# Kernel optimization log

Hardware: AMD Instinct MI355X
Metric: run time of the kernel (lower is better)

## Reference

```python
import jax, jax.numpy as jnp
import numpy as np

N, C_IN, C_OUT, T, V = 32, 4, 64, 6, 512


def setup_inputs() -> dict:
    key = jax.random.key(0)
    ks = jax.random.split(key, 8)
    x = jax.random.normal(ks[0], (N, C_IN, T, V), dtype=jnp.float32)
    # A carries 7 (unused) adjacency channels + 1 binary mask channel
    A = jax.random.randint(ks[1], (N, 8, V, V), 0, 2, dtype=jnp.int32)
    conv_w = jax.random.normal(ks[2], (C_OUT, C_IN), dtype=jnp.float32) / np.sqrt(C_IN).astype(np.float32)
    conv_b = jax.random.normal(ks[3], (C_OUT,), dtype=jnp.float32) * 0.02
    l2_w = jax.random.normal(ks[4], (1, T), dtype=jnp.float32) / np.sqrt(T).astype(np.float32)
    l2_b = jax.random.normal(ks[5], (1,), dtype=jnp.float32) * 0.02
    l1_w = jax.random.normal(ks[6], (1, 2 * C_OUT), dtype=jnp.float32) / np.sqrt(2 * C_OUT).astype(np.float32)
    l1_b = jax.random.normal(ks[7], (1,), dtype=jnp.float32) * 0.02
    return {"x": x, "A": A, "conv_w": conv_w, "conv_b": conv_b,
            "l2_w": l2_w, "l2_b": l2_b, "l1_w": l1_w, "l1_b": l1_b}


def reference(x, A, conv_w, conv_b, l2_w, l2_b, l1_w, l1_b):
    c = conv_w.shape[0]
    # 1x1 conv over (t, v): pure channel mix
    xc = jnp.einsum('nctv,oc->notv', x, conv_w) + conv_b[None, :, None, None]  # (n, 64, t, v)
    # temporal squeeze via l2: Linear(6 -> 1) on last (t) axis
    x1 = jnp.einsum('nctv,t->nvc', xc, l2_w[0]) + l2_b[0]  # (n, v, 64)
    # GAT-style pairwise score: l1(cat(x1_i, x1_j)) decomposes into two rank-1 terms
    e_i = x1 @ l1_w[0, :c]   # (n, v)
    e_j = x1 @ l1_w[0, c:]   # (n, v)
    scores = e_i[:, :, None] + e_j[:, None, :] + l1_b[0]  # (n, v, v), [n,i,j]
    scores = jnp.where(scores >= 0, scores, 0.2 * scores)  # LeakyReLU(0.2)
    # mask channel: A[:,7]; mask.long()==0 -> -inf
    mask = A[:, 7]  # (n, v, v) int
    scores = jnp.where(mask == 0, -jnp.inf, scores)
    p = jax.nn.softmax(scores, axis=2)
    p = jnp.where(jnp.isnan(p), 0.0, p)  # fully-masked rows -> 0
    # aggregate: nctv,ndvw->nctw with d=1
    out = jnp.einsum('nctv,nvw->nctw', xc, p)
    return out, p[:, None]  # (n, 64, t, v), (n, 1, v, v)
```

## Files before the change

### kernel.cpp

```cpp
#include <hip/hip_runtime.h>
#include <hip/hip_bf16.h>
#include <math.h>

#define NB   32
#define CIN  4
#define COUT 64
#define TT   6
#define VV   512
#define P_OFF (NB*COUT*TT*VV)
#define SPLITS 8
#define CH   (VV/SPLITS)
#define NROW 24
#define PKW  516

typedef __attribute__((ext_vector_type(8))) short bf16x8;
typedef __attribute__((ext_vector_type(4))) float f32x4;

__device__ inline unsigned int pack2(float a, float b) {
    __hip_bfloat162 h = __float22bfloat162_rn(make_float2(a, b));
    return *reinterpret_cast<unsigned int*>(&h);
}

__global__ __launch_bounds__(512, 4) void fused_kernel(
    const float* __restrict__ x,
    const int*   __restrict__ A,
    const float* __restrict__ conv_w,
    const float* __restrict__ conv_b,
    const float* __restrict__ l2_w,
    const float* __restrict__ l2_b,
    const float* __restrict__ l1_w,
    const float* __restrict__ l1_b,
    float*       __restrict__ p,
    float*       __restrict__ ypart)
{
    __shared__ float xst[CH][33];
    __shared__ unsigned int pk[16][PKW];
    __shared__ float W1s[CIN], W2s[CIN], cst[2], l2s[TT];
    __shared__ float ejl[VV];
    __shared__ float eil[CH];

    int s = blockIdx.x;
    int n = blockIdx.y;
    int tid = threadIdx.x;
    int lane = tid & 63;
    int q = tid >> 6;

    const int* mbase = A + (size_t)(n*8 + 7)*VV*VV;

    int4 mA0, mA1, mB0, mB1;
    {
        int i0 = s*CH + q*2;
        const int* mr = mbase + (size_t)i0*VV + lane*8;
        mA0 = *(const int4*)mr;       mA1 = *(const int4*)(mr + 4);
        mB0 = *(const int4*)(mr+VV);  mB1 = *(const int4*)(mr + VV + 4);
    }

    if (tid < CIN) {
        float w1 = 0.f, w2 = 0.f;
        for (int o = 0; o < COUT; ++o) {
            w1 += l1_w[o]        * conv_w[o*CIN + tid];
            w2 += l1_w[COUT + o] * conv_w[o*CIN + tid];
        }
        W1s[tid] = w1; W2s[tid] = w2;
    }
    if (tid < TT) l2s[tid] = l2_w[tid];
    if (tid == CIN) {
        float B1 = 0.f, B2 = 0.f, S1 = 0.f, S2 = 0.f;
        for (int o = 0; o < COUT; ++o) {
            B1 += l1_w[o]        * conv_b[o];
            B2 += l1_w[COUT + o] * conv_b[o];
            S1 += l1_w[o];
            S2 += l1_w[COUT + o];
        }
        float Ls = 0.f;
        for (int t = 0; t < TT; ++t) Ls += l2_w[t];
        cst[0] = Ls*B1 + l2_b[0]*S1;
        cst[1] = Ls*B2 + l2_b[0]*S2 + l1_b[0];
    }
    __syncthreads();

    {
        int j = tid;
        float ei = cst[0], ej = cst[1];
        #pragma unroll
        for (int c = 0; c < CIN; ++c) {
            float w1 = W1s[c], w2 = W2s[c];
            #pragma unroll
            for (int t = 0; t < TT; ++t) {
                float lw = l2s[t];
                float xv = x[((size_t)(n*CIN + c)*TT + t)*VV + j];
                ei = fmaf(lw*w1, xv, ei);
                ej = fmaf(lw*w2, xv, ej);
            }
        }
        ejl[j] = ej;
        if ((j >> 6) == s) eil[j & 63] = ei;
    }

    for (int idx = tid; idx < CH*33; idx += 512) {
        int r = idx >> 6;
        int i = idx & 63;
        float v = 0.f;
        if (r < NROW)       v = x[((size_t)n*NROW + r)*VV + s*CH + i];
        else if (r == NROW) v = 1.f;
        xst[i][r] = v;
    }
    __syncthreads();

    float ejv[8];
    #pragma unroll
    for (int m = 0; m < 8; ++m) ejv[m] = ejl[lane*8 + m];

    f32x4 acc[2][4];
    #pragma unroll
    for (int mt = 0; mt < 2; ++mt)
        #pragma unroll
        for (int t = 0; t < 4; ++t) acc[mt][t] = (f32x4){0.f, 0.f, 0.f, 0.f};

    bf16x8 afr[2][2];

    for (int sub = 0; sub < 4; ++sub) {
        int ilA  = sub*16 + q*2;
        int i_gA = s*CH + ilA;

        int4 cA0 = mA0, cA1 = mA1, cB0 = mB0, cB1 = mB1;
        float biasA = eil[ilA], biasB = eil[ilA + 1];

        if (sub < 3) {
            const int* mr = mbase + (size_t)(i_gA + 16)*VV + lane*8;
            mA0 = *(const int4*)mr;       mA1 = *(const int4*)(mr + 4);
            mB0 = *(const int4*)(mr+VV);  mB1 = *(const int4*)(mr + VV + 4);
        }

        float svA[8], svB[8];
        int mkA[8] = {cA0.x,cA0.y,cA0.z,cA0.w, cA1.x,cA1.y,cA1.z,cA1.w};
        int mkB[8] = {cB0.x,cB0.y,cB0.z,cB0.w, cB1.x,cB1.y,cB1.z,cB1.w};
        #pragma unroll
        for (int m2 = 0; m2 < 8; ++m2) {
            float tA = biasA + ejv[m2]; tA = (tA >= 0.f) ? tA : 0.2f*tA;
            svA[m2] = (mkA[m2] == 0) ? -INFINITY : tA;
            float tB = biasB + ejv[m2]; tB = (tB >= 0.f) ? tB : 0.2f*tB;
            svB[m2] = (mkB[m2] == 0) ? -INFINITY : tB;
        }
        float mA = svA[0], mB = svB[0];
        #pragma unroll
        for (int m2 = 1; m2 < 8; ++m2) {
            mA = fmaxf(mA, svA[m2]); mB = fmaxf(mB, svB[m2]);
        }
        #pragma unroll
        for (int off = 32; off; off >>= 1) {
            mA = fmaxf(mA, __shfl_xor(mA, off));
            mB = fmaxf(mB, __shfl_xor(mB, off));
        }
        float sumA = 0.f, sumB = 0.f;
        if (mA > -INFINITY) {
            #pragma unroll
            for (int m2 = 0; m2 < 8; ++m2) { svA[m2] = __expf(svA[m2]-mA); sumA += svA[m2]; }
        } else {
            #pragma unroll
            for (int m2 = 0; m2 < 8; ++m2) svA[m2] = 0.f;
        }
        if (mB > -INFINITY) {
            #pragma unroll
            for (int m2 = 0; m2 < 8; ++m2) { svB[m2] = __expf(svB[m2]-mB); sumB += svB[m2]; }
        } else {
            #pragma unroll
            for (int m2 = 0; m2 < 8; ++m2) svB[m2] = 0.f;
        }
        #pragma unroll
        for (int off = 32; off; off >>= 1) {
            sumA += __shfl_xor(sumA, off);
            sumB += __shfl_xor(sumB, off);
        }
        float invA = (sumA > 0.f) ? 1.f/sumA : 0.f;
        float invB = (sumB > 0.f) ? 1.f/sumB : 0.f;
        #pragma unroll
        for (int m2 = 0; m2 < 8; ++m2) { svA[m2] *= invA; svB[m2] *= invB; }

        float* prA = p + ((size_t)(n*VV + i_gA))*VV + lane*8;
        float4 pA03 = {svA[0],svA[1],svA[2],svA[3]}, pA47 = {svA[4],svA[5],svA[6],svA[7]};
        float4 pB03 = {svB[0],svB[1],svB[2],svB[3]}, pB47 = {svB[4],svB[5],svB[6],svB[7]};
        *(float4*)prA            = pA03;
        *(float4*)(prA + 4)      = pA47;
        *(float4*)(prA + VV)     = pB03;
        *(float4*)(prA + VV + 4) = pB47;

        {
            int pr = (sub & 1)*8 + q;
            uint4 u0 = {pack2(svA[0],svB[0]), pack2(svA[1],svB[1]),
                        pack2(svA[2],svB[2]), pack2(svA[3],svB[3])};
            uint4 u1 = {pack2(svA[4],svB[4]), pack2(svA[5],svB[5]),
                        pack2(svA[6],svB[6]), pack2(svA[7],svB[7])};
            *(uint4*)&pk[pr][lane*8]     = u0;
            *(uint4*)&pk[pr][lane*8 + 4] = u1;
        }

        if (sub & 1) {
            __syncthreads();

            if (sub == 1) {
                #pragma unroll
                for (int g = 0; g < 2; ++g)
                    #pragma unroll
                    for (int mt = 0; mt < 2; ++mt) {
                        int r  = mt*16 + (lane & 15);
                        int kb = g*32 + (lane >> 4)*8;
                        union { unsigned int u[4]; bf16x8 v; } ua;
                        #pragma unroll
                        for (int t = 0; t < 4; ++t)
                            ua.u[t] = pack2(xst[kb + 2*t][r], xst[kb + 2*t + 1][r]);
                        afr[g][mt] = ua.v;
                    }
            }

            int g = sub >> 1;
            #pragma unroll
            for (int t = 0; t < 4; ++t) {
                int ncol = (q*4 + t)*16 + (lane & 15);
                union { unsigned int u[4]; bf16x8 v; } ub;
                #pragma unroll
                for (int jj = 0; jj < 4; ++jj)
                    ub.u[jj] = pk[(lane >> 4)*4 + jj][ncol];
                acc[0][t] = __builtin_amdgcn_mfma_f32_16x16x32_bf16(afr[g][0], ub.v, acc[0][t], 0, 0, 0);
                acc[1][t] = __builtin_amdgcn_mfma_f32_16x16x32_bf16(afr[g][1], ub.v, acc[1][t], 0, 0, 0);
            }
            if (sub == 1) __syncthreads();
        }
    }

    float* yo = ypart + (size_t)(s*NB + n)*25*VV;
    #pragma unroll
    for (int mt = 0; mt < 2; ++mt)
        #pragma unroll
        for (int t = 0; t < 4; ++t) {
            int ncol = (q*4 + t)*16 + (lane & 15);
            #pragma unroll
            for (int reg = 0; reg < 4; ++reg) {
                int row = mt*16 + (lane >> 4)*4 + reg;
                if (row < 25)
                    yo[(size_t)row*VV + ncol] = acc[mt][t][reg];
            }
        }
}

__global__ __launch_bounds__(256) void expand_kernel(
    const float* __restrict__ ypart,
    const float* __restrict__ conv_w,
    const float* __restrict__ conv_b,
    float*       __restrict__ out)
{
    __shared__ float ysm[25][32];
    __shared__ float wsm[COUT*CIN];
    __shared__ float bsm[COUT];

    int wc = blockIdx.x;
    int n  = blockIdx.y;
    int tid = threadIdx.x;

    if (tid < COUT*CIN) wsm[tid] = conv_w[tid];
    if (tid < COUT)     bsm[tid] = conv_b[tid];

    for (int l4 = tid; l4 < 200; l4 += 256) {
        int r = l4 >> 3, w8 = l4 & 7;
        float4 a = {0.f, 0.f, 0.f, 0.f};
        #pragma unroll
        for (int s = 0; s < SPLITS; ++s) {
            float4 v = *(const float4*)(ypart +
                ((size_t)(s*NB + n)*25 + r)*VV + wc*32 + w8*4);
            a.x += v.x; a.y += v.y; a.z += v.z; a.w += v.w;
        }
        *(float4*)&ysm[r][w8*4] = a;
    }
    __syncthreads();

    int w  = tid & 31;
    int og = tid >> 5;

    float y[25];
    #pragma unroll
    for (int r = 0; r < 25; ++r) y[r] = ysm[r][w];

    #pragma unroll
    for (int oo = 0; oo < 8; ++oo) {
        int o = og*8 + oo;
        float wb[CIN];
        #pragma unroll
        for (int c = 0; c < CIN; ++c) wb[c] = wsm[o*CIN + c];
        float bo = bsm[o];
        #pragma unroll
        for (int t = 0; t < TT; ++t) {
            float val = bo * y[24];
            #pragma unroll
            for (int c = 0; c < CIN; ++c) val = fmaf(wb[c], y[c*TT + t], val);
            out[((size_t)(n*COUT + o)*TT + t)*VV + wc*32 + w] = val;
        }
    }
}

extern "C" void kernel_launch(void* const* d_in, const int* in_sizes, int n_in,
                              void* d_out, int out_size, void* d_ws, size_t ws_size,
                              hipStream_t stream)
{
    const float* x      = (const float*)d_in[0];
    const int*   A      = (const int*)  d_in[1];
    const float* conv_w = (const float*)d_in[2];
    const float* conv_b = (const float*)d_in[3];
    const float* l2_w   = (const float*)d_in[4];
    const float* l2_b   = (const float*)d_in[5];
    const float* l1_w   = (const float*)d_in[6];
    const float* l1_b   = (const float*)d_in[7];

    float* out = (float*)d_out;
    float* pP  = out + P_OFF;
    float* yp  = (float*)d_ws;

    dim3 gf(SPLITS, NB);
    fused_kernel<<<gf, 512, 0, stream>>>(x, A, conv_w, conv_b, l2_w, l2_b,
                                         l1_w, l1_b, pP, yp);

    dim3 ge(16, NB);
    expand_kernel<<<ge, 256, 0, stream>>>(yp, conv_w, conv_b, out);
}
```

Before: 33.60 us.

## Fuse expand kernel into main kernel via per-batch atomic counter barrier

Removes the separate expand kernel launch by having each of the 8 split blocks per batch signal completion through an atomic counter, spin-wait until all splits finish, then each block reduces the partial sums and expands two 32-column chunks of the output. This eliminates a kernel launch and its gap, but adds a memset launch and a spin-wait grid barrier that depends on all 256 blocks being co-resident. The extra shared memory may reduce occupancy.

Result: slower. 60.60 us (+80.4%).

```diff
diff --git a/kernel.cpp b/kernel.cpp
--- a/kernel.cpp
+++ b/kernel.cpp
@@ -31,13 +31,18 @@
     const float* __restrict__ l1_w,
     const float* __restrict__ l1_b,
     float*       __restrict__ p,
-    float*       __restrict__ ypart)
+    float*       __restrict__ ypart,
+    unsigned int* __restrict__ cnt,
+    float*       __restrict__ out)
 {
     __shared__ float xst[CH][33];
     __shared__ unsigned int pk[16][PKW];
     __shared__ float W1s[CIN], W2s[CIN], cst[2], l2s[TT];
     __shared__ float ejl[VV];
     __shared__ float eil[CH];
+    __shared__ float ysm[2][25][32];
+    __shared__ float wsm[COUT*CIN];
+    __shared__ float bsm[COUT];
 
     int s = blockIdx.x;
     int n = blockIdx.y;
@@ -55,6 +60,8 @@
         mB0 = *(const int4*)(mr+VV);  mB1 = *(const int4*)(mr + VV + 4);
     }
 
+    if (tid < COUT*CIN) wsm[tid] = conv_w[tid];
+    if (tid >= COUT*CIN && tid < COUT*CIN + COUT) bsm[tid - COUT*CIN] = conv_b[tid - COUT*CIN];
     if (tid < CIN) {
         float w1 = 0.f, w2 = 0.f;
         for (int o = 0; o < COUT; ++o) {
@@ -241,58 +248,56 @@
                     yo[(size_t)row*VV + ncol] = acc[mt][t][reg];
             }
         }
-}
-
-__global__ __launch_bounds__(256) void expand_kernel(
-    const float* __restrict__ ypart,
-    const float* __restrict__ conv_w,
-    const float* __restrict__ conv_b,
-    float*       __restrict__ out)
-{
-    __shared__ float ysm[25][32];
-    __shared__ float wsm[COUT*CIN];
-    __shared__ float bsm[COUT];
-
-    int wc = blockIdx.x;
-    int n  = blockIdx.y;
-    int tid = threadIdx.x;
-
-    if (tid < COUT*CIN) wsm[tid] = conv_w[tid];
-    if (tid < COUT)     bsm[tid] = conv_b[tid];
-
-    for (int l4 = tid; l4 < 200; l4 += 256) {
-        int r = l4 >> 3, w8 = l4 & 7;
-        float4 a = {0.f, 0.f, 0.f, 0.f};
-        #pragma unroll
-        for (int s = 0; s < SPLITS; ++s) {
-            float4 v = *(const float4*)(ypart +
-                ((size_t)(s*NB + n)*25 + r)*VV + wc*32 + w8*4);
-            a.x += v.x; a.y += v.y; a.z += v.z; a.w += v.w;
-        }
-        *(float4*)&ysm[r][w8*4] = a;
-    }
+
     __syncthreads();
-
-    int w  = tid & 31;
-    int og = tid >> 5;
-
-    float y[25];
-    #pragma unroll
-    for (int r = 0; r < 25; ++r) y[r] = ysm[r][w];
-
-    #pragma unroll
-    for (int oo = 0; oo < 8; ++oo) {
-        int o = og*8 + oo;
-        float wb[CIN];
-        #pragma unroll
-        for (int c = 0; c < CIN; ++c) wb[c] = wsm[o*CIN + c];
-        float bo = bsm[o];
-        #pragma unroll
-        for (int t = 0; t < TT; ++t) {
-            float val = bo * y[24];
-            #pragma unroll
-            for (int c = 0; c < CIN; ++c) val = fmaf(wb[c], y[c*TT + t], val);
-            out[((size_t)(n*COUT + o)*TT + t)*VV + wc*32 + w] = val;
+    if (tid == 0) {
+        __hip_atomic_fetch_add(&cnt[n], 1u, __ATOMIC_RELEASE,
+                               __HIP_MEMORY_SCOPE_AGENT);
+        while (__hip_atomic_load(&cnt[n], __ATOMIC_ACQUIRE,
+                                 __HIP_MEMORY_SCOPE_AGENT) < SPLITS)
+            __builtin_amdgcn_s_sleep(8);
+    }
+    __syncthreads();
+
+    {
+        int tid2 = tid & 255;
+        int half = tid >> 8;
+        int wc   = s*2 + half;
+
+        for (int l4 = tid2; l4 < 200; l4 += 256) {
+            int r = l4 >> 3, w8 = l4 & 7;
+            float4 a = {0.f, 0.f, 0.f, 0.f};
+            #pragma unroll
+            for (int s2 = 0; s2 < SPLITS; ++s2) {
+                float4 v = *(const float4*)(ypart +
+                    ((size_t)(s2*NB + n)*25 + r)*VV + wc*32 + w8*4);
+                a.x += v.x; a.y += v.y; a.z += v.z; a.w += v.w;
+            }
+            *(float4*)&ysm[half][r][w8*4] = a;
+        }
+        __syncthreads();
+
+        int w  = tid2 & 31;
+        int og = tid2 >> 5;
+
+        float y[25];
+        #pragma unroll
+        for (int r = 0; r < 25; ++r) y[r] = ysm[half][r][w];
+
+        #pragma unroll
+        for (int oo = 0; oo < 8; ++oo) {
+            int o = og*8 + oo;
+            float wb[CIN];
+            #pragma unroll
+            for (int c = 0; c < CIN; ++c) wb[c] = wsm[o*CIN + c];
+            float bo = bsm[o];
+            #pragma unroll
+            for (int t = 0; t < TT; ++t) {
+                float val = bo * y[24];
+                #pragma unroll
+                for (int c = 0; c < CIN; ++c) val = fmaf(wb[c], y[c*TT + t], val);
+                out[((size_t)(n*COUT + o)*TT + t)*VV + wc*32 + w] = val;
+            }
         }
     }
 }
@@ -313,11 +318,11 @@
     float* out = (float*)d_out;
     float* pP  = out + P_OFF;
     float* yp  = (float*)d_ws;
+    unsigned int* cnt = (unsigned int*)(yp + (size_t)SPLITS*NB*25*VV);
+
+    hipMemsetAsync(cnt, 0, NB*sizeof(unsigned int), stream);
 
     dim3 gf(SPLITS, NB);
     fused_kernel<<<gf, 512, 0, stream>>>(x, A, conv_w, conv_b, l2_w, l2_b,
-                                         l1_w, l1_b, pP, yp);
-
-    dim3 ge(16, NB);
-    expand_kernel<<<ge, 256, 0, stream>>>(yp, conv_w, conv_b, out);
+                                         l1_w, l1_b, pP, yp, cnt, out);
 }
```
